# Kernel optimization log

Measured on AMD Instinct MI355X. Metric: run time of the kernel, lower is better.

## Reference

```python
import jax, jax.numpy as jnp
import numpy as np

B, S, H, G, W_LOC = 2, 4096, 12, 64, 513  # Longformer-base: window=2*256+1, 64 global slots


def setup_inputs() -> dict:
    key = jax.random.key(0)
    k1, = jax.random.split(key, 1)
    attention_probs = jax.random.uniform(k1, (B, S, H, G + W_LOC), dtype=jnp.float32)
    attention_mask = jnp.zeros((B, S), dtype=jnp.float32)  # all tokens currently kept
    # global tokens are the first G positions of every batch; nonzero(as_tuple) index arrays
    b_idx = jnp.repeat(jnp.arange(B, dtype=jnp.int64), G)
    g_idx = jnp.tile(jnp.arange(G, dtype=jnp.int64), B)
    return {
        "attention_mask": attention_mask,
        "attention_probs": attention_probs,
        "keep_threshold": jnp.asarray(0.005, dtype=jnp.float32),  # base 0.01*6/12 + learned 0
        "max_num_global_attn_indices": G,
        "loc_b": b_idx, "loc_i": g_idx,
        "glob_b": b_idx, "glob_i": g_idx,
    }


def reference(attention_mask, attention_probs, keep_threshold,
              max_num_global_attn_indices, loc_b, loc_i, glob_b, glob_i):
    Gn = max_num_global_attn_indices
    b, s, h, wg = attention_probs.shape
    w = wg - Gn  # local window size, odd
    half = w // 2

    # zero out rows of already-masked tokens (attention_mask < 0)
    probs = jnp.where((attention_mask < 0)[:, :, None, None], 0.0, attention_probs)

    gl = probs[..., :Gn]                              # [B,S,H,G]
    lo = jnp.transpose(probs[..., Gn:], (0, 2, 1, 3))  # [B,H,S,W]

    # anti-diagonal (key-column) sums of the local band; equals the source's
    # conv2d-with-flipped-identity + slice: out[j] = sum_c lo[j + half - c, c]
    lo_p = jnp.pad(lo, ((0, 0), (0, 0), (half, half), (0, 0)))  # [B,H,S+W-1,W]
    rows = jnp.arange(s)[:, None] + (w - 1) - jnp.arange(w)[None, :]  # [S,W]
    diag = lo_p[:, :, rows, jnp.arange(w)[None, :]]  # [B,H,S,W]
    local_sum = diag.sum(axis=(1, 3))                # [B,S] (summed over heads too)

    global_sum = gl.sum(axis=(1, 2))                 # [B,G]
    probs_sum = local_sum.at[loc_b, loc_i].add(global_sum[glob_b, glob_i])

    probs_max = probs_sum.max(axis=-1, keepdims=True)
    scores = probs_sum / probs_max

    thr = jnp.maximum(jnp.float32(1e-5), jnp.asarray(keep_threshold, jnp.float32).reshape(()))
    new_attention_mask = jnp.where(scores < thr, jnp.float32(-10000.0), jnp.float32(0.0))
    return new_attention_mask, scores
```

## Files before the change

### kernel.cpp

```cpp
#include <hip/hip_runtime.h>
#include <float.h>

#define Bsz 2
#define Ssz 4096
#define Hsz 12
#define Gsz 64
#define Wsz 513
#define Csz (Gsz + Wsz)
#define ROW (Hsz * Csz)
#define HALF 256
#define RPB 8
#define NWIN (RPB - 1 + Wsz)
#define WPAD 528

#define PSUM_SZ ((size_t)Bsz * Ssz)
#define GACC_SZ ((size_t)Bsz * Gsz)

__device__ __forceinline__ int SWZ(int s) { return ((s & 3) * 132) + (s >> 2); }

__global__ __launch_bounds__(192) void k1_fused(
    const float* __restrict__ probs, const float* __restrict__ mask,
    float* __restrict__ psum, float* __restrict__ gacc)
{
    __shared__ float win[WPAD];
    const int t = threadIdx.x;
    const int row0 = blockIdx.x * RPB;
    const int b = row0 / Ssz;

    for (int u = t; u < WPAD; u += 192) win[u] = 0.f;
    __syncthreads();

    float scl[RPB];
    #pragma unroll
    for (int r = 0; r < RPB; ++r)
        scl[r] = (mask[row0 + r] < 0.f) ? 0.f : 1.f;

    const float* __restrict__ base = probs + (size_t)row0 * ROW;

    if (t < 16) {
        float ax = 0.f, ay = 0.f, az = 0.f, aw = 0.f;
        for (int r = 0; r < RPB; ++r) {
            float sx = 0.f, sy = 0.f, sz = 0.f, sw = 0.f;
            #pragma unroll
            for (int h = 0; h < Hsz; ++h) {
                float4 v = *(const float4*)(base + (size_t)r * ROW + h * Csz + 4 * t);
                sx += v.x; sy += v.y; sz += v.z; sw += v.w;
            }
            ax += sx * scl[r]; ay += sy * scl[r]; az += sz * scl[r]; aw += sw * scl[r];
        }
        atomicAdd(&gacc[b * Gsz + 4 * t + 0], ax);
        atomicAdd(&gacc[b * Gsz + 4 * t + 1], ay);
        atomicAdd(&gacc[b * Gsz + 4 * t + 2], az);
        atomicAdd(&gacc[b * Gsz + 4 * t + 3], aw);
    } else if (t < 144) {
        const int w0 = 4 * t - Gsz;
        for (int r = 0; r < RPB; ++r) {
            float sx = 0.f, sy = 0.f, sz = 0.f, sw = 0.f;
            #pragma unroll
            for (int h = 0; h < Hsz; ++h) {
                float4 v = *(const float4*)(base + (size_t)r * ROW + h * Csz + 4 * t);
                sx += v.x; sy += v.y; sz += v.z; sw += v.w;
            }
            const float sc = scl[r];
            atomicAdd(&win[SWZ(w0 + r + 0)], sx * sc);
            atomicAdd(&win[SWZ(w0 + r + 1)], sy * sc);
            atomicAdd(&win[SWZ(w0 + r + 2)], sz * sc);
            atomicAdd(&win[SWZ(w0 + r + 3)], sw * sc);
        }
    } else if (t == 144) {
        for (int r = 0; r < RPB; ++r) {
            float s = 0.f;
            #pragma unroll
            for (int h = 0; h < Hsz; ++h)
                s += base[(size_t)r * ROW + h * Csz + 576];
            atomicAdd(&win[SWZ(512 + r)], s * scl[r]);
        }
    }
    __syncthreads();

    const int s0 = row0 - b * Ssz;
    for (int w = t; w < NWIN; w += 192) {
        const int i = s0 + w - HALF;
        if (i >= 0 && i < Ssz) atomicAdd(&psum[b * Ssz + i], win[SWZ(w)]);
    }
}

__global__ __launch_bounds__(1024) void k4_final(
    const float* __restrict__ psum, const float* __restrict__ gacc,
    const float* __restrict__ thr_p,
    const int* __restrict__ loc_b, const int* __restrict__ loc_i,
    const int* __restrict__ glob_b, const int* __restrict__ glob_i,
    int n_idx, float* __restrict__ out)
{
    __shared__ float p_lds[Ssz];
    __shared__ float red[16];
    const int b = blockIdx.x;
    const int t = threadIdx.x;
    const float4* p4 = (const float4*)(psum + (size_t)b * Ssz);

    ((float4*)p_lds)[t] = p4[t];
    __syncthreads();

    if (t < n_idx && loc_b[t] == b)
        atomicAdd(&p_lds[loc_i[t]], gacc[glob_b[t] * Gsz + glob_i[t]]);
    __syncthreads();

    float m = -FLT_MAX;
    for (int i = t; i < Ssz; i += 1024) m = fmaxf(m, p_lds[i]);
    #pragma unroll
    for (int off = 32; off >= 1; off >>= 1) m = fmaxf(m, __shfl_down(m, off, 64));

    const int wave = t >> 6, lane = t & 63;
    if (lane == 0) red[wave] = m;
    __syncthreads();
    if (t == 0) {
        float mm = red[0];
        #pragma unroll
        for (int w = 1; w < 16; ++w) mm = fmaxf(mm, red[w]);
        red[0] = mm;
    }
    __syncthreads();
    const float mx = red[0];
    const float thr = fmaxf(1e-5f, thr_p[0]);

    for (int i = t; i < Ssz; i += 1024) {
        float sc = p_lds[i] / mx;
        out[(size_t)Bsz * Ssz + (size_t)b * Ssz + i] = sc;
        out[(size_t)b * Ssz + i] = (sc < thr) ? -10000.f : 0.f;
    }
}

extern "C" void kernel_launch(void* const* d_in, const int* in_sizes, int n_in,
                              void* d_out, int out_size, void* d_ws, size_t ws_size,
                              hipStream_t stream)
{
    const float* mask  = (const float*)d_in[0];
    const float* probs = (const float*)d_in[1];
    const float* thr   = (const float*)d_in[2];
    const int* loc_b  = (const int*)d_in[4];
    const int* loc_i  = (const int*)d_in[5];
    const int* glob_b = (const int*)d_in[6];
    const int* glob_i = (const int*)d_in[7];
    const int n_idx = in_sizes[4];

    float* psum = (float*)d_ws;
    float* gacc = psum + PSUM_SZ;
    float* out  = (float*)d_out;

    hipMemsetAsync(psum, 0, (PSUM_SZ + GACC_SZ) * sizeof(float), stream);

    k1_fused<<<dim3(Bsz * Ssz / RPB), dim3(192), 0, stream>>>(probs, mask, psum, gacc);
    k4_final<<<dim3(Bsz), dim3(1024), 0, stream>>>(psum, gacc, thr,
                                                   loc_b, loc_i, glob_b, glob_i,
                                                   n_idx, out);
}
```

Before: 387.2 us.

## Use aligned float4 loads across heads and register ring accumulators for window sums

Each head's 577-float segment starts at an offset that is not a multiple of four. The loads are now shifted back by (h mod 4) so every float4 read is aligned, and masks route each element to the right global or window slot. Partial anti-diagonal sums are kept in a 14-entry register ring per thread and flushed to LDS once, so the per-row shared atomics go away, along with the scalar thread that handled the last column. Global sums go through an LDS buffer before the atomics to global memory. The cost is more registers and extra multiply-by-mask work, plus __syncthreads calls placed inside divergent branches.

```diff
diff --git a/kernel.cpp b/kernel.cpp
--- a/kernel.cpp
+++ b/kernel.cpp
@@ -11,78 +11,110 @@
 #define HALF 256
 #define RPB 8
 #define NWIN (RPB - 1 + Wsz)
-#define WPAD 528
 
 #define PSUM_SZ ((size_t)Bsz * Ssz)
 #define GACC_SZ ((size_t)Bsz * Gsz)
 
-__device__ __forceinline__ int SWZ(int s) { return ((s & 3) * 132) + (s >> 2); }
-
-__global__ __launch_bounds__(192) void k1_fused(
+__global__ __launch_bounds__(192, 4) void k1_fused(
     const float* __restrict__ probs, const float* __restrict__ mask,
     float* __restrict__ psum, float* __restrict__ gacc)
 {
-    __shared__ float win[WPAD];
+    __shared__ float win[NWIN];
+    __shared__ float gl[Gsz];
     const int t = threadIdx.x;
     const int row0 = blockIdx.x * RPB;
     const int b = row0 / Ssz;
 
-    for (int u = t; u < WPAD; u += 192) win[u] = 0.f;
-    __syncthreads();
+    for (int u = t; u < NWIN; u += 192) win[u] = 0.f;
+    if (t < Gsz) gl[t] = 0.f;
 
     float scl[RPB];
     #pragma unroll
     for (int r = 0; r < RPB; ++r)
         scl[r] = (mask[row0 + r] < 0.f) ? 0.f : 1.f;
 
-    const float* __restrict__ base = probs + (size_t)row0 * ROW;
+    const float f0   = (t == 0)   ? 0.f : 1.f;
+    const float f144 = (t == 144) ? 0.f : 1.f;
+    float mp[4][4];
+    #pragma unroll
+    for (int p = 0; p < 4; ++p)
+        #pragma unroll
+        for (int j = 0; j < 4; ++j)
+            mp[p][j] = (j < p) ? f0 : ((j > p) ? f144 : 1.f);
 
-    if (t < 16) {
-        float ax = 0.f, ay = 0.f, az = 0.f, aw = 0.f;
+    float ring_w[14];
+    #pragma unroll
+    for (int s = 0; s < 14; ++s) ring_w[s] = 0.f;
+
+    const float* __restrict__ base = probs + (size_t)row0 * ROW + 4 * t;
+
+    if (t < 64) {
+        float ring_g[7];
+        float mg[7], mw[7];
+        #pragma unroll
+        for (int i = 0; i < 7; ++i) {
+            const int ch = 4 * t + i - 3;
+            ring_g[i] = 0.f;
+            mg[i] = (ch >= 0 && ch < Gsz) ? 1.f : 0.f;
+            mw[i] = 1.f - mg[i];
+        }
+        #pragma unroll
         for (int r = 0; r < RPB; ++r) {
-            float sx = 0.f, sy = 0.f, sz = 0.f, sw = 0.f;
+            const float sr = scl[r];
+            const float* rp = base + (size_t)r * ROW;
             #pragma unroll
             for (int h = 0; h < Hsz; ++h) {
-                float4 v = *(const float4*)(base + (size_t)r * ROW + h * Csz + 4 * t);
-                sx += v.x; sy += v.y; sz += v.z; sw += v.w;
+                const int p = h & 3;
+                float4 v = *(const float4*)(rp + (h * Csz - p));
+                const int ib = 3 - p;
+                const int sb = r + 3 - p;
+                float vj;
+                vj = v.x * (mp[p][0] * sr); ring_g[ib+0] += vj * mg[ib+0]; ring_w[sb+0] += vj * mw[ib+0];
+                vj = v.y * (mp[p][1] * sr); ring_g[ib+1] += vj * mg[ib+1]; ring_w[sb+1] += vj * mw[ib+1];
+                vj = v.z * (mp[p][2] * sr); ring_g[ib+2] += vj * mg[ib+2]; ring_w[sb+2] += vj * mw[ib+2];
+                vj = v.w * (mp[p][3] * sr); ring_g[ib+3] += vj * mg[ib+3]; ring_w[sb+3] += vj * mw[ib+3];
             }
-            ax += sx * scl[r]; ay += sy * scl[r]; az += sz * scl[r]; aw += sw * scl[r];
         }
-        atomicAdd(&gacc[b * Gsz + 4 * t + 0], ax);
-        atomicAdd(&gacc[b * Gsz + 4 * t + 1], ay);
-        atomicAdd(&gacc[b * Gsz + 4 * t + 2], az);
-        atomicAdd(&gacc[b * Gsz + 4 * t + 3], aw);
-    } else if (t < 144) {
-        const int w0 = 4 * t - Gsz;
+        __syncthreads();
+        #pragma unroll
+        for (int i = 0; i < 7; ++i) {
+            const int ch = 4 * t + i - 3;
+            if (ch >= 0 && ch < Gsz) atomicAdd(&gl[ch], ring_g[i]);
+        }
+    } else if (t < 145) {
+        #pragma unroll
         for (int r = 0; r < RPB; ++r) {
-            float sx = 0.f, sy = 0.f, sz = 0.f, sw = 0.f;
+            const float sr = scl[r];
+            const float* rp = base + (size_t)r * ROW;
             #pragma unroll
             for (int h = 0; h < Hsz; ++h) {
-                float4 v = *(const float4*)(base + (size_t)r * ROW + h * Csz + 4 * t);
-                sx += v.x; sy += v.y; sz += v.z; sw += v.w;
+                const int p = h & 3;
+                float4 v = *(const float4*)(rp + (h * Csz - p));
+                const int sb = r + 3 - p;
+                ring_w[sb+0] += v.x * (mp[p][0] * sr);
+                ring_w[sb+1] += v.y * (mp[p][1] * sr);
+                ring_w[sb+2] += v.z * (mp[p][2] * sr);
+                ring_w[sb+3] += v.w * (mp[p][3] * sr);
             }
-            const float sc = scl[r];
-            atomicAdd(&win[SWZ(w0 + r + 0)], sx * sc);
-            atomicAdd(&win[SWZ(w0 + r + 1)], sy * sc);
-            atomicAdd(&win[SWZ(w0 + r + 2)], sz * sc);
-            atomicAdd(&win[SWZ(w0 + r + 3)], sw * sc);
         }
-    } else if (t == 144) {
-        for (int r = 0; r < RPB; ++r) {
-            float s = 0.f;
-            #pragma unroll
-            for (int h = 0; h < Hsz; ++h)
-                s += base[(size_t)r * ROW + h * Csz + 576];
-            atomicAdd(&win[SWZ(512 + r)], s * scl[r]);
-        }
+        __syncthreads();
+    } else {
+        __syncthreads();
+    }
+
+    #pragma unroll
+    for (int s = 0; s < 14; ++s) {
+        const int w = 4 * t - 67 + s;
+        if (w >= 0 && w < NWIN) atomicAdd(&win[w], ring_w[s]);
     }
     __syncthreads();
 
     const int s0 = row0 - b * Ssz;
     for (int w = t; w < NWIN; w += 192) {
         const int i = s0 + w - HALF;
-        if (i >= 0 && i < Ssz) atomicAdd(&psum[b * Ssz + i], win[SWZ(w)]);
+        if (i >= 0 && i < Ssz) atomicAdd(&psum[b * Ssz + i], win[w]);
     }
+    if (t < Gsz) atomicAdd(&gacc[b * Gsz + t], gl[t]);
 }
 
 __global__ __launch_bounds__(1024) void k4_final(
```

New measurement: 484.8 us. 25.2% more time.
